# Kernel optimization log

Measured on AMD Instinct MI355X. Metric: run time of the kernel, lower is better.

The kernel has to match this reference:

```python
import jax, jax.numpy as jnp
import numpy as np

ALPHA = 0.2  # LeakyReLU negative slope


def gat_layer(x, W, a, alpha=ALPHA):
    """Multi-head dense GAT layer.
    x: (B, N, F); W: (H, F, O); a: (H, 2*O, 1).
    Returns (B, N, H*O) — ELU(head outputs) concatenated over heads.
    """
    H, F, O = W.shape
    Wh = jnp.einsum('bnf,hfo->bhno', x, W)          # (B,H,N,O)
    a_src = a[:, :O, 0]                              # (H,O)
    a_dst = a[:, O:, 0]                              # (H,O)
    s_src = jnp.einsum('bhno,ho->bhn', Wh, a_src)    # (B,H,N)
    s_dst = jnp.einsum('bhno,ho->bhn', Wh, a_dst)    # (B,H,N)
    e = s_src[..., :, None] + s_dst[..., None, :]    # (B,H,N,N)
    e = jax.nn.leaky_relu(e, negative_slope=alpha)
    att = jax.nn.softmax(e, axis=-1)                 # softmax over neighbors j
    out = jnp.einsum('bhnm,bhmo->bhno', att, Wh)     # (B,H,N,O)
    out = jax.nn.elu(out)
    B, _, N, _ = out.shape
    return jnp.transpose(out, (0, 2, 1, 3)).reshape(B, N, H * O)


def setup_inputs() -> dict:
    key = jax.random.key(0)
    ks = jax.random.split(key, 5)
    B, N = 32, 1024
    x = jax.random.normal(ks[0], (B, N, 4), dtype=jnp.float32)
    # layer1: nfeat=4, nhid=2, nheads=3
    W1 = jax.random.normal(ks[1], (3, 4, 2), dtype=jnp.float32) * 0.5
    a1 = jax.random.normal(ks[2], (3, 4, 1), dtype=jnp.float32) * 0.5
    # layer2: nfeat=6, nhid=4, nheads=1
    W2 = jax.random.normal(ks[3], (1, 6, 4), dtype=jnp.float32) * 0.5
    a2 = jax.random.normal(ks[4], (1, 8, 1), dtype=jnp.float32) * 0.5
    return {"x": x, "W1": W1, "a1": a1, "W2": W2, "a2": a2}


def reference(x, W1, a1, W2, a2):
    h = gat_layer(x, W1, a1)   # (B, N, 6)
    y = gat_layer(h, W2, a2)   # (B, N, 4)
    return y
```

## Files before the change

kernel.cpp:

```cpp
#include <hip/hip_runtime.h>
#include <type_traits>


#define GAT_ALPHA 0.2f
#define LOG2E 1.44269504088896f

template <int F, int O, int H>
__global__ __launch_bounds__(256) void gat_layer_kernel(
    const float* __restrict__ x,
    const float* __restrict__ Wt,
    const float* __restrict__ at,
    float* __restrict__ out)
{
    constexpr int N = 1024;
    constexpr int NT = 256;
    constexpr int RPB = 64;
    constexpr int S = 16;
    constexpr int R = 4;
    constexpr int Q = O + 1;
    constexpr int CHUNKS = N / RPB;

    const int bid   = blockIdx.x;
    const int chunk = bid & (CHUNKS - 1);
    const int h     = (bid >> 4) % H;
    const int b     = bid / (CHUNKS * H);
    const int tid   = threadIdx.x;
    const int r     = tid & 15;
    const int s     = tid >> 4;

    float Wl[F][O];
#pragma unroll
    for (int f = 0; f < F; ++f)
#pragma unroll
        for (int o = 0; o < O; ++o)
            Wl[f][o] = Wt[(h * F + f) * O + o];

    float asrc[O], adst[O];
#pragma unroll
    for (int o = 0; o < O; ++o) {
        asrc[o] = at[h * 2 * O + o];
        adst[o] = at[h * 2 * O + O + o];
    }

    __shared__ float2 sdAB[N];
    __shared__ float  sWh[N * O];
    __shared__ float  sred[4];
    __shared__ float  sredu[RPB * S * Q];
    __shared__ float  ssum[RPB * Q];

    const float* xb = x + (size_t)b * N * F;
    float dmax = -3.0e38f;
    for (int m = tid; m < N; m += NT) {
        float xv[F];
#pragma unroll
        for (int f = 0; f < F; ++f) xv[f] = xb[(size_t)m * F + f];
        float d = 0.0f;
#pragma unroll
        for (int o = 0; o < O; ++o) {
            float wh = 0.0f;
#pragma unroll
            for (int f = 0; f < F; ++f) wh += xv[f] * Wl[f][o];
            sWh[m * O + o] = wh;
            d += wh * adst[o];
        }
        sdAB[m] = make_float2(d * LOG2E, d * (GAT_ALPHA * LOG2E));
        dmax = fmaxf(dmax, d);
    }
#pragma unroll
    for (int off = 32; off > 0; off >>= 1)
        dmax = fmaxf(dmax, __shfl_xor(dmax, off, 64));
    if ((tid & 63) == 0) sred[tid >> 6] = dmax;
    __syncthreads();
    const float D = fmaxf(fmaxf(sred[0], sred[1]), fmaxf(sred[2], sred[3]));

    float t1[R], t2[R];
#pragma unroll
    for (int j = 0; j < R; ++j) {
        const int row = chunk * RPB + r + 16 * j;
        float sn = 0.0f;
#pragma unroll
        for (int o = 0; o < O; ++o) sn += sWh[row * O + o] * asrc[o];
        const float e0m = sn + D;
        const float eM  = fmaxf(e0m, GAT_ALPHA * e0m);
        t1[j] = (sn - eM) * LOG2E;
        t2[j] = (GAT_ALPHA * sn - eM) * LOG2E;
    }

    float den[R];
    float num[R][O];
#pragma unroll
    for (int j = 0; j < R; ++j) {
        den[j] = 0.0f;
#pragma unroll
        for (int o = 0; o < O; ++o) num[j][o] = 0.0f;
    }

    using WVec = typename std::conditional<O == 2, float2, float4>::type;
    const WVec* sWhV = (const WVec*)sWh;

#pragma unroll 4
    for (int mi = 0; mi < N / S; ++mi) {
        const int m = mi * S + s;
        const float2 ab = sdAB[m];
        const WVec  wv = sWhV[m];
        const float* wp = (const float*)&wv;
#pragma unroll
        for (int j = 0; j < R; ++j) {
            const float arg = fmaxf(ab.x + t1[j], ab.y + t2[j]);
            const float w   = __builtin_amdgcn_exp2f(arg);
            den[j] += w;
#pragma unroll
            for (int o = 0; o < O; ++o) num[j][o] += w * wp[o];
        }
    }

#pragma unroll
    for (int j = 0; j < R; ++j) {
        float* p = &sredu[(((s * 16) + r) * R + j) * Q];
        p[0] = den[j];
#pragma unroll
        for (int o = 0; o < O; ++o) p[1 + o] = num[j][o];
    }
    __syncthreads();

    for (int idx = tid; idx < RPB * Q; idx += NT) {
        const int rowl = idx / Q, q = idx % Q;
        const int rr = rowl & 15, jj = rowl >> 4;
        float acc = 0.0f;
#pragma unroll
        for (int ss = 0; ss < S; ++ss)
            acc += sredu[(((ss * 16) + rr) * R + jj) * Q + q];
        ssum[rowl * Q + q] = acc;
    }
    __syncthreads();

    for (int idx = tid; idx < RPB * O; idx += NT) {
        const int rowl = idx / O, o = idx % O;
        const float inv = 1.0f / ssum[rowl * Q];
        float v = ssum[rowl * Q + 1 + o] * inv;
        v = (v > 0.0f) ? v : (__expf(v) - 1.0f);
        const int row = chunk * RPB + rowl;
        out[((size_t)b * N + row) * (H * O) + h * O + o] = v;
    }
}

extern "C" void kernel_launch(void* const* d_in, const int* in_sizes, int n_in,
                              void* d_out, int out_size, void* d_ws, size_t ws_size,
                              hipStream_t stream) {
    const float* x  = (const float*)d_in[0];
    const float* W1 = (const float*)d_in[1];
    const float* a1 = (const float*)d_in[2];
    const float* W2 = (const float*)d_in[3];
    const float* a2 = (const float*)d_in[4];

    float* h1 = (float*)d_ws;
    float* y  = (float*)d_out;

    constexpr int B = 32;
    gat_layer_kernel<4, 2, 3><<<B * 3 * 16, 256, 0, stream>>>(x, W1, a1, h1);
    gat_layer_kernel<6, 4, 1><<<B * 1 * 16, 256, 0, stream>>>(h1, W2, a2, y);
}
```

Measured before the change: 97.77 us.

## Factor exponentials into per-column and per-row terms, removing exp from inner loop

Rewrites the softmax weight exp2(max(a+t1,b+t2)) as a per-column precomputed exp pair times a per-row constant, selected by comparing d_m against -s_n, so the inner N×R loop carries no transcendental. Doubles rows per block (RPB 128, R 8), halving grid size and the redundant per-block Wh projection. It also transposes the partial-sum reduction layout and vectorizes the x loads. Risks: lower block count on a large GPU, more registers, and possible underflow when a tiny exp term is multiplied by a tiny row constant.

Result: faster. 93.14 us (-4.7%).

```diff
diff --git a/kernel.cpp b/kernel.cpp
--- a/kernel.cpp
+++ b/kernel.cpp
@@ -1,5 +1,4 @@
 #include <hip/hip_runtime.h>
-#include <type_traits>
 
 
 #define GAT_ALPHA 0.2f
@@ -12,17 +11,13 @@
     const float* __restrict__ at,
     float* __restrict__ out)
 {
-    constexpr int N = 1024;
-    constexpr int NT = 256;
-    constexpr int RPB = 64;
-    constexpr int S = 16;
-    constexpr int R = 4;
+    constexpr int N = 1024, NT = 256, RPB = 128, S = 16, R = 8;
+    constexpr int CHUNKS = N / RPB;
     constexpr int Q = O + 1;
-    constexpr int CHUNKS = N / RPB;
 
     const int bid   = blockIdx.x;
-    const int chunk = bid & (CHUNKS - 1);
-    const int h     = (bid >> 4) % H;
+    const int chunk = bid % CHUNKS;
+    const int h     = (bid / CHUNKS) % H;
     const int b     = bid / (CHUNKS * H);
     const int tid   = threadIdx.x;
     const int r     = tid & 15;
@@ -42,18 +37,27 @@
         adst[o] = at[h * 2 * O + O + o];
     }
 
-    __shared__ float2 sdAB[N];
-    __shared__ float  sWh[N * O];
+    __shared__ __align__(16) float sWh[N * O];
+    __shared__ float2 sE[N];
+    __shared__ float  sdp[N];
     __shared__ float  sred[4];
-    __shared__ float  sredu[RPB * S * Q];
+    __shared__ float  sredu[RPB * Q * S];
     __shared__ float  ssum[RPB * Q];
 
     const float* xb = x + (size_t)b * N * F;
     float dmax = -3.0e38f;
     for (int m = tid; m < N; m += NT) {
         float xv[F];
+        if constexpr (F == 4) {
+            const float4 v = ((const float4*)xb)[m];
+            xv[0] = v.x; xv[1] = v.y; xv[2] = v.z; xv[3] = v.w;
+        } else {
 #pragma unroll
-        for (int f = 0; f < F; ++f) xv[f] = xb[(size_t)m * F + f];
+            for (int k = 0; k < F / 2; ++k) {
+                const float2 v = ((const float2*)xb)[m * (F / 2) + k];
+                xv[2 * k] = v.x; xv[2 * k + 1] = v.y;
+            }
+        }
         float d = 0.0f;
 #pragma unroll
         for (int o = 0; o < O; ++o) {
@@ -63,7 +67,7 @@
             sWh[m * O + o] = wh;
             d += wh * adst[o];
         }
-        sdAB[m] = make_float2(d * LOG2E, d * (GAT_ALPHA * LOG2E));
+        sdp[m] = d;
         dmax = fmaxf(dmax, d);
     }
 #pragma unroll
@@ -73,21 +77,28 @@
     __syncthreads();
     const float D = fmaxf(fmaxf(sred[0], sred[1]), fmaxf(sred[2], sred[3]));
 
-    float t1[R], t2[R];
+    for (int m = tid; m < N; m += NT) {
+        const float t = (sdp[m] - D) * LOG2E;
+        sE[m] = make_float2(__builtin_amdgcn_exp2f(t),
+                            __builtin_amdgcn_exp2f(GAT_ALPHA * t));
+    }
+
+    float thr[R], c1[R], c2[R];
 #pragma unroll
     for (int j = 0; j < R; ++j) {
         const int row = chunk * RPB + r + 16 * j;
         float sn = 0.0f;
 #pragma unroll
         for (int o = 0; o < O; ++o) sn += sWh[row * O + o] * asrc[o];
-        const float e0m = sn + D;
-        const float eM  = fmaxf(e0m, GAT_ALPHA * e0m);
-        t1[j] = (sn - eM) * LOG2E;
-        t2[j] = (GAT_ALPHA * sn - eM) * LOG2E;
+        const float z = sn + D;
+        const float e = __builtin_amdgcn_exp2f(-0.8f * LOG2E * fabsf(z));
+        c1[j] = (z >= 0.0f) ? 1.0f : e;
+        c2[j] = (z >= 0.0f) ? e : 1.0f;
+        thr[j] = -sn;
     }
+    __syncthreads();
 
-    float den[R];
-    float num[R][O];
+    float den[R], num[R][O];
 #pragma unroll
     for (int j = 0; j < R; ++j) {
         den[j] = 0.0f;
@@ -95,19 +106,22 @@
         for (int o = 0; o < O; ++o) num[j][o] = 0.0f;
     }
 
-    using WVec = typename std::conditional<O == 2, float2, float4>::type;
-    const WVec* sWhV = (const WVec*)sWh;
-
 #pragma unroll 4
     for (int mi = 0; mi < N / S; ++mi) {
         const int m = mi * S + s;
-        const float2 ab = sdAB[m];
-        const WVec  wv = sWhV[m];
-        const float* wp = (const float*)&wv;
+        const float  dm = sdp[m];
+        const float2 E  = sE[m];
+        float wp[O];
+        if constexpr (O == 2) {
+            const float2 wv = ((const float2*)sWh)[m];
+            wp[0] = wv.x; wp[1] = wv.y;
+        } else {
+            const float4 wv = ((const float4*)sWh)[m];
+            wp[0] = wv.x; wp[1] = wv.y; wp[2] = wv.z; wp[3] = wv.w;
+        }
 #pragma unroll
         for (int j = 0; j < R; ++j) {
-            const float arg = fmaxf(ab.x + t1[j], ab.y + t2[j]);
-            const float w   = __builtin_amdgcn_exp2f(arg);
+            const float w = (dm >= thr[j]) ? (c1[j] * E.x) : (c2[j] * E.y);
             den[j] += w;
 #pragma unroll
             for (int o = 0; o < O; ++o) num[j][o] += w * wp[o];
@@ -116,21 +130,19 @@
 
 #pragma unroll
     for (int j = 0; j < R; ++j) {
-        float* p = &sredu[(((s * 16) + r) * R + j) * Q];
-        p[0] = den[j];
+        const int rowl = r + 16 * j;
+        sredu[(rowl * Q + 0) * S + s] = den[j];
 #pragma unroll
-        for (int o = 0; o < O; ++o) p[1 + o] = num[j][o];
+        for (int o = 0; o < O; ++o)
+            sredu[(rowl * Q + 1 + o) * S + s] = num[j][o];
     }
     __syncthreads();
 
     for (int idx = tid; idx < RPB * Q; idx += NT) {
-        const int rowl = idx / Q, q = idx % Q;
-        const int rr = rowl & 15, jj = rowl >> 4;
         float acc = 0.0f;
 #pragma unroll
-        for (int ss = 0; ss < S; ++ss)
-            acc += sredu[(((ss * 16) + rr) * R + jj) * Q + q];
-        ssum[rowl * Q + q] = acc;
+        for (int ss = 0; ss < S; ++ss) acc += sredu[idx * S + ss];
+        ssum[idx] = acc;
     }
     __syncthreads();
 
@@ -157,6 +169,6 @@
     float* y  = (float*)d_out;
 
     constexpr int B = 32;
-    gat_layer_kernel<4, 2, 3><<<B * 3 * 16, 256, 0, stream>>>(x, W1, a1, h1);
-    gat_layer_kernel<6, 4, 1><<<B * 1 * 16, 256, 0, stream>>>(h1, W2, a2, y);
+    gat_layer_kernel<4, 2, 3><<<B * 3 * 8, 256, 0, stream>>>(x, W1, a1, h1);
+    gat_layer_kernel<6, 4, 1><<<B * 1 * 8, 256, 0, stream>>>(h1, W2, a2, y);
 }
```
